# Kernel tuning notes

Hardware: AMD Instinct MI355X
Metric: run time of the kernel (lower is better)

Reference implementation:

```python
import jax, jax.numpy as jnp
import numpy as np

B, H, W = 8, 64, 64
DIM, HEADS, WS = 512, 8, 8
C2 = DIM // 2            # attention branch channels
HD = C2 // HEADS         # head dim = 32
NH, NW = H // WS, W // WS
WIN = WS * WS            # tokens per window = 64
SCALE = HD ** -0.5
EPS = 1e-5


def layer_norm(x, g, b):
    m = jnp.mean(x, axis=-1, keepdims=True)
    v = jnp.mean((x - m) ** 2, axis=-1, keepdims=True)
    return (x - m) * jax.lax.rsqrt(v + EPS) * g + b


def dwconv3x3(x, w, b=None):
    # x: (N, C, h, w); w: (C, 1, 3, 3) depthwise
    out = jax.lax.conv_general_dilated(
        x, w, window_strides=(1, 1), padding='SAME',
        feature_group_count=x.shape[1],
        dimension_numbers=('NCHW', 'OIHW', 'NCHW'))
    if b is not None:
        out = out + b[None, :, None, None]
    return out


def setup_inputs() -> dict:
    key = jax.random.key(0)
    ks = jax.random.split(key, 8)
    r = lambda k, s: (jax.random.normal(k, s, jnp.float32) * 0.02)
    return {
        'x': jax.random.normal(ks[0], (B, H * W, DIM), jnp.float32),
        'norm1_g': jnp.ones((DIM,), jnp.float32),
        'norm1_b': jnp.zeros((DIM,), jnp.float32),
        'qkv_w': r(ks[1], (C2, 3 * C2)),
        'qkv_b': jnp.zeros((3 * C2,), jnp.float32),
        'lepe_w': r(ks[2], (C2, 1, 3, 3)),
        'lepe_b': jnp.zeros((C2,), jnp.float32),
        'convloc_w': r(ks[3], (C2, 1, 3, 3)),
        'proj_w': r(ks[4], (DIM, DIM)),
        'proj_b': jnp.zeros((DIM,), jnp.float32),
        'norm2_g': jnp.ones((DIM,), jnp.float32),
        'norm2_b': jnp.zeros((DIM,), jnp.float32),
        'fc1_w': r(ks[5], (DIM, 4 * DIM)),
        'fc1_b': jnp.zeros((4 * DIM,), jnp.float32),
        'fc2_w': r(ks[6], (4 * DIM, DIM)),
        'fc2_b': jnp.zeros((DIM,), jnp.float32),
    }


def reference(x, norm1_g, norm1_b, qkv_w, qkv_b, lepe_w, lepe_b, convloc_w,
              proj_w, proj_b, norm2_g, norm2_b, fc1_w, fc1_b, fc2_w, fc2_b):
    img = layer_norm(x, norm1_g, norm1_b)                      # (B, L, DIM)

    # qkv from first half of channels
    qkv = img[..., :C2] @ qkv_w + qkv_b                        # (B, L, 3*C2)
    qkv = qkv.reshape(B, H * W, 3, C2)
    q, k, v = qkv[:, :, 0], qkv[:, :, 1], qkv[:, :, 2]

    def win6(t):  # (B, L, C2) -> (B, NH, NW, WS, WS, C2)
        return t.reshape(B, NH, WS, NW, WS, C2).transpose(0, 1, 3, 2, 4, 5)

    def to_heads(t6):
        return t6.reshape(-1, WIN, HEADS, HD).transpose(0, 2, 1, 3)

    qh = to_heads(win6(q)) * SCALE
    kh = to_heads(win6(k))

    # v + LePE: depthwise 3x3 conv applied per-window
    vw = win6(v).transpose(0, 1, 2, 5, 3, 4).reshape(-1, C2, WS, WS)
    lepe = dwconv3x3(vw, lepe_w, lepe_b)                       # (nWin, C2, WS, WS)
    vh = vw.reshape(-1, HEADS, HD, WIN).transpose(0, 1, 3, 2)
    leh = lepe.reshape(-1, HEADS, HD, WIN).transpose(0, 1, 3, 2)

    attn = jax.nn.softmax(jnp.einsum('nhqd,nhkd->nhqk', qh, kh), axis=-1)
    o = jnp.einsum('nhqk,nhkd->nhqd', attn, vh) + leh

    # merge windows back to (B, L, C2)
    o = o.transpose(0, 2, 1, 3).reshape(B, NH, NW, WS, WS, C2)
    o = o.transpose(0, 1, 3, 2, 4, 5).reshape(B, H * W, C2)

    # parallel depthwise-conv branch on second half of channels (no bias)
    x2 = img[..., C2:].transpose(0, 2, 1).reshape(B, C2, H, W)
    x2 = dwconv3x3(x2, convloc_w)
    x2 = x2.reshape(B, C2, H * W).transpose(0, 2, 1)

    local = jnp.concatenate([o, x2], axis=-1) @ proj_w + proj_b
    x = x + local

    # MLP_FFN: Linear -> GELU -> Linear
    h = jax.nn.gelu(layer_norm(x, norm2_g, norm2_b) @ fc1_w + fc1_b,
                    approximate=False)
    x = x + (h @ fc2_w + fc2_b)
    return x
```

## Files before the change

kernel.cpp:

```cpp
#include <hip/hip_runtime.h>
#include <cstdint>
#include <cstddef>

typedef unsigned short u16;
typedef __attribute__((ext_vector_type(8))) short short8;
typedef __attribute__((ext_vector_type(4))) float f32x4;

#define DIM 512
#define C2  256
#define HD  32
#define SCALE_Q 0.17677669529663689f

__device__ __forceinline__ float bf2f(u16 u){ return __uint_as_float(((unsigned)u) << 16); }
__device__ __forceinline__ u16 f2bf(float f){
  unsigned u = __float_as_uint(f);
  unsigned r = (u + 0x7FFFu + ((u >> 16) & 1u)) >> 16;
  return (u16)r;
}

__device__ __forceinline__ f32x4 mfma16(short8 a, short8 b, f32x4 c){
  return __builtin_amdgcn_mfma_f32_16x16x32_bf16(a, b, c, 0, 0, 0);
}

__device__ __forceinline__ void gload16(const u16* g, u16* l){
  __builtin_amdgcn_global_load_lds((const __attribute__((address_space(1))) void*)g,
                                   (__attribute__((address_space(3))) void*)l, 16, 0, 0);
}

__device__ __forceinline__ float gelu_f(float v){
  float e = __expf(-1.702f * v);
  return v * __builtin_amdgcn_rcpf(1.0f + e);
}

__global__ __launch_bounds__(256) void transpose_kernel(const float* __restrict__ W,
                                                        u16* __restrict__ WT, int K, int N){
  __shared__ u16 Tl[32][33];
  int n0 = blockIdx.x * 32, k0 = blockIdx.y * 32;
  int tx = threadIdx.x & 31, ty = threadIdx.x >> 5;
#pragma unroll
  for (int i = 0; i < 4; i++){
    int k = ty * 4 + i;
    Tl[k][tx] = f2bf(W[(size_t)(k0 + k) * N + n0 + tx]);
  }
  __syncthreads();
#pragma unroll
  for (int i = 0; i < 4; i++){
    int n = ty * 4 + i;
    WT[(size_t)(n0 + n) * K + k0 + tx] = Tl[tx][n];
  }
}

__global__ __launch_bounds__(256) void ln_kernel(const float* __restrict__ x, const float* __restrict__ g,
                                                 const float* __restrict__ bta, u16* __restrict__ out){
  int row  = blockIdx.x * 4 + (threadIdx.x >> 6);
  int lane = threadIdx.x & 63;
  size_t base = (size_t)row * DIM + lane * 8;
  float4 v0 = *(const float4*)(x + base);
  float4 v1 = *(const float4*)(x + base + 4);
  float f[8] = {v0.x, v0.y, v0.z, v0.w, v1.x, v1.y, v1.z, v1.w};
  float s = 0.f;
#pragma unroll
  for (int j = 0; j < 8; j++) s += f[j];
#pragma unroll
  for (int m = 1; m < 64; m <<= 1) s += __shfl_xor(s, m, 64);
  float mean = s * (1.0f / DIM);
  float vs = 0.f;
#pragma unroll
  for (int j = 0; j < 8; j++){ float d = f[j] - mean; vs += d * d; }
#pragma unroll
  for (int m = 1; m < 64; m <<= 1) vs += __shfl_xor(vs, m, 64);
  float rstd = rsqrtf(vs * (1.0f / DIM) + 1e-5f);
  float4 g0 = *(const float4*)(g + lane * 8);
  float4 g1 = *(const float4*)(g + lane * 8 + 4);
  float4 b0 = *(const float4*)(bta + lane * 8);
  float4 b1 = *(const float4*)(bta + lane * 8 + 4);
  float gg[8] = {g0.x, g0.y, g0.z, g0.w, g1.x, g1.y, g1.z, g1.w};
  float bb[8] = {b0.x, b0.y, b0.z, b0.w, b1.x, b1.y, b1.z, b1.w};
  short8 o;
#pragma unroll
  for (int j = 0; j < 8; j++){
    float r = (f[j] - mean) * rstd * gg[j] + bb[j];
    o[j] = (short)f2bf(r);
  }
  *(short8*)(out + base) = o;
}

template<int EPI, bool OUT_BF16>
__global__ __launch_bounds__(512, 2) void gemm8_kernel(
    const u16* __restrict__ A, int lda,
    const u16* __restrict__ WT,
    const float* __restrict__ bias,
    const float* R, int ldr,
    void* Cv, int ldc, int K)
{
  __shared__ u16 Al[2][2][256 * 32];
  __shared__ u16 Bl[2][2][256 * 32];
  const int tid = threadIdx.x;
  const int l   = tid & 63;
  const int w   = tid >> 6;
  const int wr  = w >> 2;
  const int wc  = w & 3;
  const int l16 = l & 15, lhi = l >> 4;

  const int gx = gridDim.x;
  int bid = blockIdx.y * gx + blockIdx.x;
  int nwg = gx * gridDim.y;
  int sw  = (nwg & 7) ? bid : ((bid & 7) * (nwg >> 3) + (bid >> 3));
  const int col0 = (sw % gx) * 256, row0 = (sw / gx) * 256;
  const int NT = K >> 6;

  const int srow = w * 16 + (l >> 2);
  const int cs   = (((l & 3) ^ ((l >> 3) & 3)) * 8);
  const u16* pA = A  + (size_t)(row0 + srow) * lda + cs;
  const u16* pB = WT + (size_t)(col0 + srow) * K  + cs;
  const size_t a128 = (size_t)128 * lda, b128 = (size_t)128 * K;

  auto stageA = [&](int tt, int hh){
    if (tt < NT){
      size_t go = (size_t)tt * 64 + (size_t)hh * 32;
      gload16(pA + go,        &Al[tt & 1][hh][(w * 16) * 32]);
      gload16(pA + a128 + go, &Al[tt & 1][hh][(128 + w * 16) * 32]);
    }
  };
  auto stageB = [&](int tt, int hh){
    if (tt < NT){
      size_t go = (size_t)tt * 64 + (size_t)hh * 32;
      gload16(pB + go,        &Bl[tt & 1][hh][(w * 16) * 32]);
      gload16(pB + b128 + go, &Bl[tt & 1][hh][(128 + w * 16) * 32]);
    }
  };

  const int rdo = l16 * 32 + (lhi ^ ((l16 >> 1) & 3)) * 8;

  f32x4 acc[8][4] = {};
  short8 af[4], bf[4];

  stageA(0, 0); stageB(0, 0); stageA(0, 1); stageB(0, 1);
  stageA(1, 0); stageB(1, 0); stageA(1, 1); stageB(1, 1);
  asm volatile("s_waitcnt vmcnt(8)" ::: "memory");
  __builtin_amdgcn_sched_barrier(0);
  __builtin_amdgcn_s_barrier();

#define PHASE(BC, KH, QM, STAGES) do{                                                   \
    if ((QM) == 0){                                                                     \
      _Pragma("unroll")                                                                 \
      for (int n = 0; n < 4; n++)                                                       \
        bf[n] = *(const short8*)&Bl[BC][KH][(wc * 64 + n * 16) * 32 + rdo];             \
    }                                                                                   \
    _Pragma("unroll")                                                                   \
    for (int m = 0; m < 4; m++)                                                         \
      af[m] = *(const short8*)&Al[BC][KH][(wr * 128 + (QM) * 64 + m * 16) * 32 + rdo];  \
    STAGES;                                                                             \
    __builtin_amdgcn_s_barrier();                                                       \
    asm volatile("s_waitcnt lgkmcnt(0)" ::: "memory");                                  \
    __builtin_amdgcn_sched_barrier(0);                                                  \
    __builtin_amdgcn_s_setprio(1);                                                      \
    _Pragma("unroll")                                                                   \
    for (int m = 0; m < 4; m++)                                                         \
      _Pragma("unroll")                                                                 \
      for (int n = 0; n < 4; n++)                                                       \
        acc[(QM) * 4 + m][n] = mfma16(bf[n], af[m], acc[(QM) * 4 + m][n]);              \
    __builtin_amdgcn_s_setprio(0);                                                      \
    __builtin_amdgcn_s_barrier();                                                       \
  }while(0)

  for (int t = 0; t < NT; t++){
    const int bc = t & 1;
    PHASE(bc, 0, 0, (void)0);
    PHASE(bc, 0, 1, stageB(t + 2, 0));
    PHASE(bc, 1, 0, stageA(t + 2, 0));
    PHASE(bc, 1, 1, stageB(t + 2, 1));
    stageA(t + 2, 1);
    if (t + 2 < NT) asm volatile("s_waitcnt vmcnt(8)" ::: "memory");
    else            asm volatile("s_waitcnt vmcnt(0)" ::: "memory");
    __builtin_amdgcn_sched_barrier(0);
    __builtin_amdgcn_s_barrier();
  }
#undef PHASE

  float4 bvs[4];
#pragma unroll
  for (int n = 0; n < 4; n++)
    bvs[n] = *(const float4*)&bias[col0 + wc * 64 + n * 16 + lhi * 4];
#pragma unroll
  for (int mq = 0; mq < 8; mq++){
    int grow = row0 + wr * 128 + mq * 16 + l16;
#pragma unroll
    for (int n = 0; n < 4; n++){
      int gcol = col0 + wc * 64 + n * 16 + lhi * 4;
      float4 vv = { acc[mq][n][0] + bvs[n].x, acc[mq][n][1] + bvs[n].y,
                    acc[mq][n][2] + bvs[n].z, acc[mq][n][3] + bvs[n].w };
      if constexpr (EPI == 1){
        float4 rv = *(const float4*)&R[(size_t)grow * ldr + gcol];
        vv.x += rv.x; vv.y += rv.y; vv.z += rv.z; vv.w += rv.w;
      }
      if constexpr (EPI == 2){
        vv.x = gelu_f(vv.x); vv.y = gelu_f(vv.y); vv.z = gelu_f(vv.z); vv.w = gelu_f(vv.w);
      }
      if constexpr (OUT_BF16){
        ushort4 o4 = { f2bf(vv.x), f2bf(vv.y), f2bf(vv.z), f2bf(vv.w) };
        *(ushort4*)&((u16*)Cv)[(size_t)grow * ldc + gcol] = o4;
      } else {
        *(float4*)&((float*)Cv)[(size_t)grow * ldc + gcol] = vv;
      }
    }
  }
}

__global__ __launch_bounds__(64) void attn_kernel(
    const u16* __restrict__ qkv, const float* __restrict__ lw,
    const float* __restrict__ lb, u16* __restrict__ out)
{
  __shared__ float Ks[64][33];
  __shared__ float Vs[64][33];
  __shared__ float Wle[32][9];
  __shared__ float Lb[32];
  int head = blockIdx.x & 7, win = blockIdx.x >> 3;
  int wx = win & 7, wy = (win >> 3) & 7, b = win >> 6;
  int l  = threadIdx.x;
  int py = l >> 3, px = l & 7;
  size_t t = (size_t)b * 4096 + (size_t)(wy * 8 + py) * 64 + (wx * 8 + px);
  const u16* base = qkv + t * 768 + head * HD;

  float q[32];
#pragma unroll
  for (int j = 0; j < 32; j += 8){
    short8 vq = *(const short8*)(base + j);
    short8 vk = *(const short8*)(base + 256 + j);
    short8 vv = *(const short8*)(base + 512 + j);
#pragma unroll
    for (int e = 0; e < 8; e++){
      q[j + e]     = bf2f((u16)vq[e]) * SCALE_Q;
      Ks[l][j + e] = bf2f((u16)vk[e]);
      Vs[l][j + e] = bf2f((u16)vv[e]);
    }
  }
  for (int i = l; i < 288; i += 64) Wle[i / 9][i % 9] = lw[(head * 32 + i / 9) * 9 + (i % 9)];
  if (l < 32) Lb[l] = lb[head * 32 + l];
  __syncthreads();

  float sc[64];
  float mx = -1e30f;
#pragma unroll
  for (int k = 0; k < 64; k++){
    float s = 0.f;
#pragma unroll
    for (int d = 0; d < 32; d++) s += q[d] * Ks[k][d];
    sc[k] = s; mx = fmaxf(mx, s);
  }
  float sum = 0.f;
#pragma unroll
  for (int k = 0; k < 64; k++){ float e = __expf(sc[k] - mx); sc[k] = e; sum += e; }
  float inv = 1.0f / sum;
  float o[32];
#pragma unroll
  for (int d = 0; d < 32; d++) o[d] = 0.f;
#pragma unroll
  for (int k = 0; k < 64; k++){
    float p = sc[k] * inv;
#pragma unroll
    for (int d = 0; d < 32; d++) o[d] += p * Vs[k][d];
  }
#pragma unroll
  for (int ky = 0; ky < 3; ky++){
    int yy = py + ky - 1;
    if (yy < 0 || yy >= 8) continue;
#pragma unroll
    for (int kx = 0; kx < 3; kx++){
      int xx = px + kx - 1;
      if (xx < 0 || xx >= 8) continue;
      int kp = yy * 8 + xx;
#pragma unroll
      for (int d = 0; d < 32; d++) o[d] += Wle[d][ky * 3 + kx] * Vs[kp][d];
    }
  }
  u16* op = out + t * DIM + head * HD;
#pragma unroll
  for (int d = 0; d < 32; d += 4){
    ushort4 o4 = { f2bf(o[d] + Lb[d]), f2bf(o[d + 1] + Lb[d + 1]),
                   f2bf(o[d + 2] + Lb[d + 2]), f2bf(o[d + 3] + Lb[d + 3]) };
    *(ushort4*)&op[d] = o4;
  }
}

__global__ __launch_bounds__(256) void convloc_kernel(const u16* __restrict__ img,
    const float* __restrict__ w, u16* __restrict__ out){
  int c  = threadIdx.x;
  int pg = blockIdx.x;
  int b  = pg >> 8;
  int p0 = (pg & 255) * 16;
  float wt[9];
#pragma unroll
  for (int i = 0; i < 9; i++) wt[i] = w[c * 9 + i];
  for (int pi = 0; pi < 16; pi++){
    int p = p0 + pi;
    int y = p >> 6, x = p & 63;
    float acc = 0.f;
#pragma unroll
    for (int ky = 0; ky < 3; ky++){
      int yy = y + ky - 1;
      if (yy < 0 || yy >= 64) continue;
#pragma unroll
      for (int kx = 0; kx < 3; kx++){
        int xx = x + kx - 1;
        if (xx < 0 || xx >= 64) continue;
        acc += wt[ky * 3 + kx] * bf2f(img[((size_t)b * 4096 + yy * 64 + xx) * DIM + C2 + c]);
      }
    }
    out[((size_t)b * 4096 + p) * DIM + C2 + c] = f2bf(acc);
  }
}

extern "C" void kernel_launch(void* const* d_in, const int* in_sizes, int n_in,
                              void* d_out, int out_size, void* d_ws, size_t ws_size,
                              hipStream_t stream){
  const float* x      = (const float*)d_in[0];
  const float* n1g    = (const float*)d_in[1];
  const float* n1b    = (const float*)d_in[2];
  const float* qkv_w  = (const float*)d_in[3];
  const float* qkv_b  = (const float*)d_in[4];
  const float* lepe_w = (const float*)d_in[5];
  const float* lepe_b = (const float*)d_in[6];
  const float* conv_w = (const float*)d_in[7];
  const float* proj_w = (const float*)d_in[8];
  const float* proj_b = (const float*)d_in[9];
  const float* n2g    = (const float*)d_in[10];
  const float* n2b    = (const float*)d_in[11];
  const float* fc1_w  = (const float*)d_in[12];
  const float* fc1_b  = (const float*)d_in[13];
  const float* fc2_w  = (const float*)d_in[14];
  const float* fc2_b  = (const float*)d_in[15];
  float* out = (float*)d_out;

  char* ws = (char*)d_ws;
  u16* img     = (u16*)(ws + 0);
  u16* qkvb    = (u16*)(ws + 33554432ull);
  u16* localb  = (u16*)(ws + 83886080ull);
  u16* y       = (u16*)(ws + 0);
  u16* h       = (u16*)(ws + 33554432ull);
  u16* qkv_wT  = (u16*)(ws + 167772160ull);
  u16* proj_wT = (u16*)(ws + 167772160ull + 393216ull);
  u16* fc1_wT  = (u16*)(ws + 167772160ull + 393216ull + 524288ull);
  u16* fc2_wT  = (u16*)(ws + 167772160ull + 393216ull + 524288ull + 2097152ull);
  float* xa    = (float*)d_out;

  { dim3 g(24, 8);  transpose_kernel<<<g, 256, 0, stream>>>(qkv_w,  qkv_wT,  256, 768);  }
  { dim3 g(16, 16); transpose_kernel<<<g, 256, 0, stream>>>(proj_w, proj_wT, 512, 512);  }
  { dim3 g(64, 16); transpose_kernel<<<g, 256, 0, stream>>>(fc1_w,  fc1_wT,  512, 2048); }
  { dim3 g(16, 64); transpose_kernel<<<g, 256, 0, stream>>>(fc2_w,  fc2_wT,  2048, 512); }

  ln_kernel<<<8192, 256, 0, stream>>>(x, n1g, n1b, img);

  dim3 gq(3, 128);
  gemm8_kernel<0, true><<<gq, 512, 0, stream>>>(img, DIM, qkv_wT, qkv_b, nullptr, 0, qkvb, 768, 256);

  attn_kernel<<<4096, 64, 0, stream>>>(qkvb, lepe_w, lepe_b, localb);
  convloc_kernel<<<2048, 256, 0, stream>>>(img, conv_w, localb);

  dim3 gp(2, 128);
  gemm8_kernel<1, false><<<gp, 512, 0, stream>>>(localb, DIM, proj_wT, proj_b, x, DIM, xa, DIM, 512);

  ln_kernel<<<8192, 256, 0, stream>>>(xa, n2g, n2b, y);

  dim3 g1(8, 128);
  gemm8_kernel<2, true><<<g1, 512, 0, stream>>>(y, DIM, fc1_wT, fc1_b, nullptr, 0, h, 2048, 512);

  dim3 g2(2, 128);
  gemm8_kernel<1, false><<<g2, 512, 0, stream>>>(h, 2048, fc2_wT, fc2_b, xa, DIM, out, DIM, 2048);
}
```

Before: 444.6 us.

## Fuse proj GEMM with residual and LayerNorm2; merge weight transposes into one launch

Adds a proj GEMM kernel in which each block owns 128 full rows of the 512-wide output, so the residual add and the second LayerNorm are computed in the epilogue through a cross-wave shared-memory reduction. This removes the separate LN2 pass, which re-read the fp32 residual stream. The four weight-transpose launches are also merged into a single launch. In exchange the proj kernel runs only 256 blocks with one row-tile each, which lowers parallelism, and it computes variance as E[x²]−mean², which is less numerically robust.

Result: slower. 457.6 us (+2.9%).

```diff
diff --git a/kernel.cpp b/kernel.cpp
--- a/kernel.cpp
+++ b/kernel.cpp
@@ -32,10 +32,19 @@
   return v * __builtin_amdgcn_rcpf(1.0f + e);
 }
 
-__global__ __launch_bounds__(256) void transpose_kernel(const float* __restrict__ W,
-                                                        u16* __restrict__ WT, int K, int N){
+__global__ __launch_bounds__(256) void transpose_all_kernel(
+    const float* __restrict__ qkv_w, const float* __restrict__ proj_w,
+    const float* __restrict__ fc1_w, const float* __restrict__ fc2_w,
+    u16* __restrict__ qkv_wT, u16* __restrict__ proj_wT,
+    u16* __restrict__ fc1_wT, u16* __restrict__ fc2_wT){
   __shared__ u16 Tl[32][33];
-  int n0 = blockIdx.x * 32, k0 = blockIdx.y * 32;
+  int b = blockIdx.x;
+  const float* W; u16* WT; int K, N, nx, ti;
+  if (b < 192)      { W = qkv_w;  WT = qkv_wT;  K = 256;  N = 768;  nx = 24; ti = b; }
+  else if (b < 448) { W = proj_w; WT = proj_wT; K = 512;  N = 512;  nx = 16; ti = b - 192; }
+  else if (b < 1472){ W = fc1_w;  WT = fc1_wT;  K = 512;  N = 2048; nx = 64; ti = b - 448; }
+  else              { W = fc2_w;  WT = fc2_wT;  K = 2048; N = 512;  nx = 16; ti = b - 1472; }
+  int n0 = (ti % nx) * 32, k0 = (ti / nx) * 32;
   int tx = threadIdx.x & 31, ty = threadIdx.x >> 5;
 #pragma unroll
   for (int i = 0; i < 4; i++){
@@ -86,7 +95,7 @@
 }
 
 template<int EPI, bool OUT_BF16>
-__global__ __launch_bounds__(512, 2) void gemm8_kernel(
+__device__ __forceinline__ void gemm8_body(
     const u16* __restrict__ A, int lda,
     const u16* __restrict__ WT,
     const float* __restrict__ bias,
@@ -207,6 +216,139 @@
   }
 }
 
+__global__ __launch_bounds__(512, 2) void gemm_qkv_kernel(const u16* A, int lda, const u16* WT,
+    const float* bias, const float* R, int ldr, void* Cv, int ldc, int K){
+  gemm8_body<0, true>(A, lda, WT, bias, R, ldr, Cv, ldc, K);
+}
+__global__ __launch_bounds__(512, 2) void gemm_fc1_kernel(const u16* A, int lda, const u16* WT,
+    const float* bias, const float* R, int ldr, void* Cv, int ldc, int K){
+  gemm8_body<2, true>(A, lda, WT, bias, R, ldr, Cv, ldc, K);
+}
+__global__ __launch_bounds__(512, 2) void gemm_fc2_kernel(const u16* A, int lda, const u16* WT,
+    const float* bias, const float* R, int ldr, void* Cv, int ldc, int K){
+  gemm8_body<1, false>(A, lda, WT, bias, R, ldr, Cv, ldc, K);
+}
+
+__global__ __launch_bounds__(512, 2) void proj_ln2_kernel(
+    const u16* __restrict__ A,
+    const u16* __restrict__ WT,
+    const float* __restrict__ bias,
+    const float* __restrict__ X,
+    const float* __restrict__ g2, const float* __restrict__ b2,
+    float* __restrict__ xa, u16* __restrict__ y)
+{
+  __shared__ u16 Al[2][128 * 32];
+  __shared__ u16 Bl[2][512 * 32];
+  __shared__ float Sred[2][4][128];
+  const int tid = threadIdx.x;
+  const int l   = tid & 63;
+  const int w   = tid >> 6;
+  const int wr  = w >> 2;
+  const int wc  = w & 3;
+  const int l16 = l & 15, lhi = l >> 4;
+
+  int bid = blockIdx.x, nwg = gridDim.x;
+  int sw  = (nwg & 7) ? bid : ((bid & 7) * (nwg >> 3) + (bid >> 3));
+  const int row0 = sw * 128;
+  const int NT = 16;
+
+  const int cs = (((l & 3) ^ ((l >> 3) & 3)) * 8);
+  const u16* pA = A  + (size_t)(row0 + w * 16 + (l >> 2)) * DIM + cs;
+  const u16* pB = WT + (size_t)(w * 64 + (l >> 2)) * DIM + cs;
+
+  auto stage = [&](int tt){
+    if (tt < NT){
+      size_t go = (size_t)tt * 32;
+      gload16(pA + go, &Al[tt & 1][(w * 16) * 32]);
+#pragma unroll
+      for (int j = 0; j < 4; j++)
+        gload16(pB + go + (size_t)j * 16 * DIM, &Bl[tt & 1][(w * 64 + j * 16) * 32]);
+    }
+  };
+
+  const int rdo = l16 * 32 + (lhi ^ ((l16 >> 1) & 3)) * 8;
+
+  f32x4 acc[4][8] = {};
+
+  stage(0);
+  __syncthreads();
+  for (int t = 0; t < NT; t++){
+    stage(t + 1);
+    __builtin_amdgcn_sched_barrier(0);
+    const int cur = t & 1;
+    short8 af[4], bf[8];
+#pragma unroll
+    for (int n = 0; n < 8; n++)
+      bf[n] = *(const short8*)&Bl[cur][(wc * 128 + n * 16) * 32 + rdo];
+#pragma unroll
+    for (int m = 0; m < 4; m++)
+      af[m] = *(const short8*)&Al[cur][(wr * 64 + m * 16) * 32 + rdo];
+    __builtin_amdgcn_s_setprio(1);
+#pragma unroll
+    for (int m = 0; m < 4; m++)
+#pragma unroll
+      for (int n = 0; n < 8; n++)
+        acc[m][n] = mfma16(bf[n], af[m], acc[m][n]);
+    __builtin_amdgcn_s_setprio(0);
+    __syncthreads();
+  }
+
+  float psum[4] = {0,0,0,0}, psq[4] = {0,0,0,0};
+#pragma unroll
+  for (int m = 0; m < 4; m++){
+    int grow = row0 + wr * 64 + m * 16 + l16;
+#pragma unroll
+    for (int n = 0; n < 8; n++){
+      int gcol = wc * 128 + n * 16 + lhi * 4;
+      float4 bb = *(const float4*)&bias[gcol];
+      float4 rv = *(const float4*)&X[(size_t)grow * DIM + gcol];
+      f32x4 v = acc[m][n];
+      v[0] += bb.x + rv.x; v[1] += bb.y + rv.y; v[2] += bb.z + rv.z; v[3] += bb.w + rv.w;
+      acc[m][n] = v;
+      float4 o = { v[0], v[1], v[2], v[3] };
+      *(float4*)&xa[(size_t)grow * DIM + gcol] = o;
+      psum[m] += v[0] + v[1] + v[2] + v[3];
+      psq[m]  += v[0]*v[0] + v[1]*v[1] + v[2]*v[2] + v[3]*v[3];
+    }
+  }
+#pragma unroll
+  for (int m = 0; m < 4; m++){
+    psum[m] += __shfl_xor(psum[m], 16, 64); psum[m] += __shfl_xor(psum[m], 32, 64);
+    psq[m]  += __shfl_xor(psq[m],  16, 64); psq[m]  += __shfl_xor(psq[m],  32, 64);
+  }
+  if (lhi == 0){
+#pragma unroll
+    for (int m = 0; m < 4; m++){
+      int br = wr * 64 + m * 16 + l16;
+      Sred[0][wc][br] = psum[m];
+      Sred[1][wc][br] = psq[m];
+    }
+  }
+  __syncthreads();
+#pragma unroll
+  for (int m = 0; m < 4; m++){
+    int br = wr * 64 + m * 16 + l16;
+    int grow = row0 + br;
+    float s = Sred[0][0][br] + Sred[0][1][br] + Sred[0][2][br] + Sred[0][3][br];
+    float q = Sred[1][0][br] + Sred[1][1][br] + Sred[1][2][br] + Sred[1][3][br];
+    float mean = s * (1.0f / DIM);
+    float var  = q * (1.0f / DIM) - mean * mean;
+    float rstd = rsqrtf(var + 1e-5f);
+#pragma unroll
+    for (int n = 0; n < 8; n++){
+      int gcol = wc * 128 + n * 16 + lhi * 4;
+      float4 gg  = *(const float4*)&g2[gcol];
+      float4 b2v = *(const float4*)&b2[gcol];
+      f32x4 v = acc[m][n];
+      ushort4 o4 = { f2bf((v[0] - mean) * rstd * gg.x + b2v.x),
+                     f2bf((v[1] - mean) * rstd * gg.y + b2v.y),
+                     f2bf((v[2] - mean) * rstd * gg.z + b2v.z),
+                     f2bf((v[3] - mean) * rstd * gg.w + b2v.w) };
+      *(ushort4*)&y[(size_t)grow * DIM + gcol] = o4;
+    }
+  }
+}
+
 __global__ __launch_bounds__(64) void attn_kernel(
     const u16* __restrict__ qkv, const float* __restrict__ lw,
     const float* __restrict__ lb, u16* __restrict__ out)
@@ -344,27 +486,22 @@
   u16* fc2_wT  = (u16*)(ws + 167772160ull + 393216ull + 524288ull + 2097152ull);
   float* xa    = (float*)d_out;
 
-  { dim3 g(24, 8);  transpose_kernel<<<g, 256, 0, stream>>>(qkv_w,  qkv_wT,  256, 768);  }
-  { dim3 g(16, 16); transpose_kernel<<<g, 256, 0, stream>>>(proj_w, proj_wT, 512, 512);  }
-  { dim3 g(64, 16); transpose_kernel<<<g, 256, 0, stream>>>(fc1_w,  fc1_wT,  512, 2048); }
-  { dim3 g(16, 64); transpose_kernel<<<g, 256, 0, stream>>>(fc2_w,  fc2_wT,  2048, 512); }
+  transpose_all_kernel<<<2496, 256, 0, stream>>>(qkv_w, proj_w, fc1_w, fc2_w,
+                                                 qkv_wT, proj_wT, fc1_wT, fc2_wT);
 
   ln_kernel<<<8192, 256, 0, stream>>>(x, n1g, n1b, img);
 
   dim3 gq(3, 128);
-  gemm8_kernel<0, true><<<gq, 512, 0, stream>>>(img, DIM, qkv_wT, qkv_b, nullptr, 0, qkvb, 768, 256);
+  gemm_qkv_kernel<<<gq, 512, 0, stream>>>(img, DIM, qkv_wT, qkv_b, nullptr, 0, qkvb, 768, 256);
 
   attn_kernel<<<4096, 64, 0, stream>>>(qkvb, lepe_w, lepe_b, localb);
   convloc_kernel<<<2048, 256, 0, stream>>>(img, conv_w, localb);
 
-  dim3 gp(2, 128);
-  gemm8_kernel<1, false><<<gp, 512, 0, stream>>>(localb, DIM, proj_wT, proj_b, x, DIM, xa, DIM, 512);
-
-  ln_kernel<<<8192, 256, 0, stream>>>(xa, n2g, n2b, y);
+  proj_ln2_kernel<<<256, 512, 0, stream>>>(localb, proj_wT, proj_b, x, n2g, n2b, xa, y);
 
   dim3 g1(8, 128);
-  gemm8_kernel<2, true><<<g1, 512, 0, stream>>>(y, DIM, fc1_wT, fc1_b, nullptr, 0, h, 2048, 512);
+  gemm_fc1_kernel<<<g1, 512, 0, stream>>>(y, DIM, fc1_wT, fc1_b, nullptr, 0, h, 2048, 512);
 
   dim3 g2(2, 128);
-  gemm8_kernel<1, false><<<g2, 512, 0, stream>>>(h, 2048, fc2_wT, fc2_b, xa, DIM, out, DIM, 2048);
-}
+  gemm_fc2_kernel<<<g2, 512, 0, stream>>>(h, 2048, fc2_wT, fc2_b, xa, DIM, out, DIM, 2048);
+}
```
